# Optimization experiments

Hardware: AMD Instinct MI355X
Metric: run time of the kernel (lower is better)

## Reference

```python
import jax, jax.numpy as jnp
import numpy as np

EPS = 1e-5
H = 1024  # hidden_size
IN = 1024  # input_size
B = 4096


def _layer_norm(x, gamma, beta):
    mu = jnp.mean(x, axis=-1, keepdims=True)
    var = jnp.mean(jnp.square(x - mu), axis=-1, keepdims=True)
    return (x - mu) * jax.lax.rsqrt(var + EPS) * gamma + beta


def setup_inputs() -> dict:
    key = jax.random.key(0)
    ks = jax.random.split(key, 8)
    s_h = 1.0 / np.sqrt(H)
    s_x = 1.0 / np.sqrt(IN)
    return {
        "x": jax.random.normal(ks[0], (B, IN), dtype=jnp.float32),
        "h": jax.random.normal(ks[1], (B, H), dtype=jnp.float32),
        "c": jax.random.normal(ks[2], (B, H), dtype=jnp.float32),
        # hidden_lin: Linear(H, 4H) with bias; input_lin: Linear(IN, 4H) no bias
        "W_h": jax.random.uniform(ks[3], (H, 4 * H), jnp.float32, -s_h, s_h),
        "b_h": jax.random.uniform(ks[4], (4 * H,), jnp.float32, -s_h, s_h),
        "W_x": jax.random.uniform(ks[5], (IN, 4 * H), jnp.float32, -s_x, s_x),
        # 4 gate LayerNorms stacked [4,H], plus LayerNorm for c
        "ln_g": jnp.ones((4, H), jnp.float32),
        "ln_b": jnp.zeros((4, H), jnp.float32),
        "lnc_g": jnp.ones((H,), jnp.float32),
        "lnc_b": jnp.zeros((H,), jnp.float32),
    }


def reference(x, h, c, W_h, b_h, W_x, ln_g, ln_b, lnc_g, lnc_b):
    # ifgo = hidden_lin(h) + input_lin(x) : [B, 4H]
    ifgo = h @ W_h + b_h + x @ W_x
    ifgo = ifgo.reshape(x.shape[0], 4, H)  # [B, 4, H]
    ifgo = _layer_norm(ifgo, ln_g, ln_b)   # per-gate LayerNorm over last dim
    i, f, g, o = ifgo[:, 0], ifgo[:, 1], ifgo[:, 2], ifgo[:, 3]
    c_next = jax.nn.sigmoid(f) * c + jax.nn.sigmoid(i) * jnp.tanh(g)
    h_next = jax.nn.sigmoid(o) * jnp.tanh(_layer_norm(c_next, lnc_g, lnc_b))
    return (h_next, c_next)
```

## Files before the change

kernel.cpp:

```cpp
#include <hip/hip_runtime.h>

typedef short bf16x8 __attribute__((ext_vector_type(8)));
typedef unsigned short u16x8 __attribute__((ext_vector_type(8)));
typedef float f32x4  __attribute__((ext_vector_type(4)));

__device__ __forceinline__ float bf2f(unsigned short u) {
  union { unsigned int i; float f; } x; x.i = ((unsigned int)u) << 16; return x.f;
}
__device__ __forceinline__ unsigned short f2bf(float f) {
  union { float f; unsigned int i; } x; x.f = f;
  unsigned int r = x.i + 0x7fffu + ((x.i >> 16) & 1u);
  return (unsigned short)(r >> 16);
}
__device__ __forceinline__ float sigm(float v) { return 1.f / (1.f + __expf(-v)); }
__device__ __forceinline__ float tanh_(float v) { return 1.f - 2.f / (__expf(2.f * v) + 1.f); }
__device__ __forceinline__ int is_fp32(const void* lng) {
  return ((*(const unsigned int*)lng) & 0xFFFFu) == 0u;
}

#define AS1 __attribute__((address_space(1)))
#define AS3 __attribute__((address_space(3)))

__global__ __launch_bounds__(256) void prep_kernel(
    const void* __restrict__ h, const void* __restrict__ x,
    const void* __restrict__ Wh, const void* __restrict__ Wx,
    const void* __restrict__ lng,
    unsigned short* __restrict__ Ap, unsigned short* __restrict__ Wt)
{
  __shared__ unsigned short tile[64][65];
  const int fp = is_fp32(lng);
  if (blockIdx.x < 4096) {
    const int row = blockIdx.x;
    const int col = threadIdx.x * 8;
    const void* src; int sc;
    if (col < 1024) { src = h; sc = col; } else { src = x; sc = col - 1024; }
    u16x8 o;
    if (fp) {
      const float* s = (const float*)src + (size_t)row * 1024 + sc;
      float4 a = *(const float4*)s;
      float4 b = *(const float4*)(s + 4);
      o[0] = f2bf(a.x); o[1] = f2bf(a.y); o[2] = f2bf(a.z); o[3] = f2bf(a.w);
      o[4] = f2bf(b.x); o[5] = f2bf(b.y); o[6] = f2bf(b.z); o[7] = f2bf(b.w);
    } else {
      o = *(const u16x8*)((const unsigned short*)src + (size_t)row * 1024 + sc);
    }
    *(u16x8*)(Ap + (size_t)row * 2048 + col) = o;
  } else {
    const int bid = blockIdx.x - 4096;
    const int n0 = (bid & 63) * 64;
    const int k0 = (bid >> 6) * 64;
    const int tx = threadIdx.x & 63;
    const int ty = threadIdx.x >> 6;
    const void* src; int krow;
    if (k0 < 1024) { src = Wh; krow = k0; } else { src = Wx; krow = k0 - 1024; }
#pragma unroll
    for (int i = 0; i < 16; ++i) {
      int kk = ty + i * 4;
      size_t idx = (size_t)(krow + kk) * 4096 + n0 + tx;
      tile[kk][tx] = fp ? f2bf(((const float*)src)[idx])
                        : ((const unsigned short*)src)[idx];
    }
    __syncthreads();
#pragma unroll
    for (int i = 0; i < 16; ++i) {
      int nn = ty + i * 4;
      Wt[(size_t)(n0 + nn) * 2048 + k0 + tx] = tile[tx][nn];
    }
  }
}


#define BAR()   __builtin_amdgcn_s_barrier()
#define SBAR()  __builtin_amdgcn_sched_barrier(0)
#define LGKM0() { asm volatile("s_waitcnt lgkmcnt(0)" ::: "memory"); SBAR(); }
#define VMW(N)  { asm volatile("s_waitcnt vmcnt(" #N ")" ::: "memory"); }

#define LOAD_A(DB, MH)                                                         \
  { const unsigned short* _ba = &As[DB][(MH)*128 + wr*64 + fr][0];             \
    _Pragma("unroll") for (int mi = 0; mi < 4; ++mi)                           \
      _Pragma("unroll") for (int kh = 0; kh < 2; ++kh)                         \
        a[mi][kh] = *(const bf16x8*)(_ba + mi*1024 + ((kh*4 + fq) ^ xk) * 8); }

#define LOAD_B(DB, NH)                                                         \
  { const unsigned short* _bb = &Bs[DB][(NH)*128 + wc*32 + fr][0];             \
    _Pragma("unroll") for (int ni = 0; ni < 2; ++ni)                           \
      _Pragma("unroll") for (int kh = 0; kh < 2; ++kh)                         \
        b[ni][kh] = *(const bf16x8*)(_bb + ni*1024 + ((kh*4 + fq) ^ xk) * 8); }

#define MFMA16(MH, NH)                                                         \
  { __builtin_amdgcn_s_setprio(1);                                             \
    _Pragma("unroll") for (int kh = 0; kh < 2; ++kh)                           \
      _Pragma("unroll") for (int mi = 0; mi < 4; ++mi)                         \
        _Pragma("unroll") for (int ni = 0; ni < 2; ++ni)                       \
          acc[MH][mi][NH][ni] = __builtin_amdgcn_mfma_f32_16x16x32_bf16(       \
              a[mi][kh], b[ni][kh], acc[MH][mi][NH][ni], 0, 0, 0);             \
    __builtin_amdgcn_s_setprio(0); }

#define STAGE(G, LDS, ROW0, H, KT)                                             \
  { _Pragma("unroll") for (int l = 0; l < 2; ++l) {                            \
      const int _idx = l * 512 + tid;                                          \
      const int _r = _idx >> 3;                                                \
      const int _sg = (_idx & 7) ^ (_r & 7);                                   \
      const unsigned short* _src = (G) + (size_t)((ROW0) + (H)*128 + _r) * 2048\
                                   + ((KT) << 6) + _sg * 8;                    \
      __builtin_amdgcn_global_load_lds((const AS1 void*)_src,                  \
          (AS3 void*)(&(LDS)[0][0] + (H)*8192 + (l*512 + wave*64)*8), 16, 0, 0);\
  } }

__global__ __launch_bounds__(512, 2) void gemm_kernel(
    const unsigned short* __restrict__ Ap,
    const unsigned short* __restrict__ Wt,
    unsigned short* __restrict__ Cout)
{
  __shared__ __align__(16) unsigned short As[2][256][64];
  __shared__ __align__(16) unsigned short Bs[2][256][64];

  const int bid = blockIdx.x;
  const int swz = (bid & 7) * 32 + (bid >> 3);
  const int bm = swz >> 4, bn = swz & 15;
  const int arow = bm * 256, brow = bn * 256;

  const int tid  = threadIdx.x;
  const int wave = tid >> 6, lane = tid & 63;
  const int wr = wave >> 2, wc = wave & 3;
  const int fr = lane & 15, fq = lane >> 4;
  const int xk = fr & 7;

  f32x4 acc[2][4][2][2] = {};
  bf16x8 a[4][2], b[2][2];

  STAGE(Ap, As[0], arow, 0, 0);
  STAGE(Ap, As[0], arow, 1, 0);
  STAGE(Wt, Bs[0], brow, 0, 0);
  STAGE(Wt, Bs[0], brow, 1, 0);
  STAGE(Wt, Bs[1], brow, 0, 1);
  STAGE(Ap, As[1], arow, 1, 1);
  VMW(4);
  SBAR(); BAR();

#pragma unroll 1
  for (int it = 0; it < 16; ++it) {
    const int t1 = (2 * it + 1) & 31;
    const int t2 = (2 * it + 2) & 31;
    const int t3 = (2 * it + 3) & 31;

    LOAD_A(0, 0) LOAD_B(0, 0)
    STAGE(Ap, As[1], arow, 0, t1);
    SBAR(); BAR(); LGKM0();
    MFMA16(0, 0);
    SBAR(); BAR();
    LOAD_A(0, 1)
    STAGE(Wt, Bs[1], brow, 1, t1);
    SBAR(); BAR(); LGKM0();
    MFMA16(1, 0);
    SBAR(); BAR();
    LOAD_B(0, 1)
    STAGE(Wt, Bs[0], brow, 0, t2);
    SBAR(); BAR(); LGKM0();
    MFMA16(1, 1);
    SBAR(); BAR();
    LOAD_A(0, 0)
    STAGE(Ap, As[0], arow, 1, t2);
    SBAR(); BAR(); LGKM0();
    MFMA16(0, 1);
    VMW(4);
    SBAR(); BAR();
    LOAD_A(1, 0) LOAD_B(1, 0)
    STAGE(Ap, As[0], arow, 0, t2);
    SBAR(); BAR(); LGKM0();
    MFMA16(0, 0);
    SBAR(); BAR();
    LOAD_A(1, 1)
    STAGE(Wt, Bs[0], brow, 1, t2);
    SBAR(); BAR(); LGKM0();
    MFMA16(1, 0);
    SBAR(); BAR();
    LOAD_B(1, 1)
    STAGE(Wt, Bs[1], brow, 0, t3);
    SBAR(); BAR(); LGKM0();
    MFMA16(1, 1);
    SBAR(); BAR();
    LOAD_A(1, 0)
    STAGE(Ap, As[1], arow, 1, t3);
    SBAR(); BAR(); LGKM0();
    MFMA16(0, 1);
    VMW(4);
    SBAR(); BAR();
  }
  VMW(0);

  unsigned short* Cb = Cout + (size_t)arow * 4096 + brow;
#pragma unroll
  for (int mh = 0; mh < 2; ++mh)
#pragma unroll
    for (int mi = 0; mi < 4; ++mi)
#pragma unroll
      for (int nh = 0; nh < 2; ++nh)
#pragma unroll
        for (int ni = 0; ni < 2; ++ni) {
          const int row = mh * 128 + wr * 64 + mi * 16 + fq * 4;
          const int col = nh * 128 + wc * 32 + ni * 16 + fr;
#pragma unroll
          for (int r = 0; r < 4; ++r)
            Cb[(size_t)(row + r) * 4096 + col] = f2bf(acc[mh][mi][nh][ni][r]);
        }
}

__device__ __forceinline__ float4 load4(const void* p, size_t idx, int fp) {
  if (fp) return *(const float4*)((const float*)p + idx);
  ushort4 u = *(const ushort4*)((const unsigned short*)p + idx);
  return make_float4(bf2f(u.x), bf2f(u.y), bf2f(u.z), bf2f(u.w));
}
__device__ __forceinline__ void store4(void* p, size_t idx, int fp,
                                       float a, float b, float c, float d) {
  if (fp) {
    *(float4*)((float*)p + idx) = make_float4(a, b, c, d);
  } else {
    ushort4 u; u.x = f2bf(a); u.y = f2bf(b); u.z = f2bf(c); u.w = f2bf(d);
    *(ushort4*)((unsigned short*)p + idx) = u;
  }
}

__global__ __launch_bounds__(256) void ln_lstm_kernel(
    const unsigned short* __restrict__ parts,
    const void* __restrict__ c,
    const void* __restrict__ bh,
    const void* __restrict__ ln_g,
    const void* __restrict__ ln_b,
    const void* __restrict__ lnc_g,
    const void* __restrict__ lnc_b,
    void* __restrict__ out)
{
  const int b = blockIdx.x;
  const int t = threadIdx.x;
  const int lane = t & 63, wave = t >> 6;
  const int fp = is_fp32(lnc_g);
  const unsigned short* P0 = parts + (size_t)b * 4096;

  __shared__ float sred[4][8];

  float v[4][4];
  float red[8];
#pragma unroll
  for (int q = 0; q < 4; ++q) {
    ushort4 p0 = *(const ushort4*)(P0 + q * 1024 + t * 4);
    float4 b4 = load4(bh, q * 1024 + t * 4, fp);
    v[q][0] = bf2f(p0.x) + b4.x;
    v[q][1] = bf2f(p0.y) + b4.y;
    v[q][2] = bf2f(p0.z) + b4.z;
    v[q][3] = bf2f(p0.w) + b4.w;
    red[q * 2]     = v[q][0] + v[q][1] + v[q][2] + v[q][3];
    red[q * 2 + 1] = v[q][0]*v[q][0] + v[q][1]*v[q][1] + v[q][2]*v[q][2] + v[q][3]*v[q][3];
  }
#pragma unroll
  for (int j = 0; j < 8; ++j) {
    float s = red[j];
#pragma unroll
    for (int off = 32; off > 0; off >>= 1) s += __shfl_down(s, off, 64);
    if (lane == 0) sred[wave][j] = s;
  }
  __syncthreads();
  float mu[4], rs[4];
#pragma unroll
  for (int q = 0; q < 4; ++q) {
    float s  = sred[0][2*q]   + sred[1][2*q]   + sred[2][2*q]   + sred[3][2*q];
    float sq = sred[0][2*q+1] + sred[1][2*q+1] + sred[2][2*q+1] + sred[3][2*q+1];
    mu[q] = s * (1.f / 1024.f);
    float var = sq * (1.f / 1024.f) - mu[q] * mu[q];
    rs[q] = rsqrtf(var + 1e-5f);
  }

  float4 gI = load4(ln_g, 0 * 1024 + t * 4, fp), bI = load4(ln_b, 0 * 1024 + t * 4, fp);
  float4 gF = load4(ln_g, 1 * 1024 + t * 4, fp), bF = load4(ln_b, 1 * 1024 + t * 4, fp);
  float4 gG = load4(ln_g, 2 * 1024 + t * 4, fp), bG = load4(ln_b, 2 * 1024 + t * 4, fp);
  float4 gO = load4(ln_g, 3 * 1024 + t * 4, fp), bO = load4(ln_b, 3 * 1024 + t * 4, fp);
  float gg[4][4] = { {gI.x,gI.y,gI.z,gI.w}, {gF.x,gF.y,gF.z,gF.w},
                     {gG.x,gG.y,gG.z,gG.w}, {gO.x,gO.y,gO.z,gO.w} };
  float gb[4][4] = { {bI.x,bI.y,bI.z,bI.w}, {bF.x,bF.y,bF.z,bF.w},
                     {bG.x,bG.y,bG.z,bG.w}, {bO.x,bO.y,bO.z,bO.w} };

  float4 c4 = load4(c, (size_t)b * 1024 + t * 4, fp);
  float cin[4] = { c4.x, c4.y, c4.z, c4.w };

  float cn[4], osg[4];
  float csum = 0.f, csq = 0.f;
#pragma unroll
  for (int e = 0; e < 4; ++e) {
    float iv = (v[0][e] - mu[0]) * rs[0] * gg[0][e] + gb[0][e];
    float fv = (v[1][e] - mu[1]) * rs[1] * gg[1][e] + gb[1][e];
    float gv = (v[2][e] - mu[2]) * rs[2] * gg[2][e] + gb[2][e];
    float ov = (v[3][e] - mu[3]) * rs[3] * gg[3][e] + gb[3][e];
    float cne = sigm(fv) * cin[e] + sigm(iv) * tanh_(gv);
    cn[e] = cne; csum += cne; csq += cne * cne;
    osg[e] = sigm(ov);
  }
  store4(out, (size_t)4096 * 1024 + (size_t)b * 1024 + t * 4, fp, cn[0], cn[1], cn[2], cn[3]);

  __syncthreads();
  {
    float s0 = csum, s1 = csq;
#pragma unroll
    for (int off = 32; off > 0; off >>= 1) { s0 += __shfl_down(s0, off, 64); s1 += __shfl_down(s1, off, 64); }
    if (lane == 0) { sred[wave][0] = s0; sred[wave][1] = s1; }
  }
  __syncthreads();
  float cs   = sred[0][0] + sred[1][0] + sred[2][0] + sred[3][0];
  float csq2 = sred[0][1] + sred[1][1] + sred[2][1] + sred[3][1];
  float mu_c = cs * (1.f / 1024.f);
  float var_c = csq2 * (1.f / 1024.f) - mu_c * mu_c;
  float rs_c = rsqrtf(var_c + 1e-5f);

  float4 cg4 = load4(lnc_g, t * 4, fp);
  float4 cb4 = load4(lnc_b, t * 4, fp);

  float hn[4];
  float cgv[4] = { cg4.x, cg4.y, cg4.z, cg4.w };
  float cbv[4] = { cb4.x, cb4.y, cb4.z, cb4.w };
#pragma unroll
  for (int e = 0; e < 4; ++e)
    hn[e] = osg[e] * tanh_((cn[e] - mu_c) * rs_c * cgv[e] + cbv[e]);
  store4(out, (size_t)b * 1024 + t * 4, fp, hn[0], hn[1], hn[2], hn[3]);
}

extern "C" void kernel_launch(void* const* d_in, const int* in_sizes, int n_in,
                              void* d_out, int out_size, void* d_ws, size_t ws_size,
                              hipStream_t stream) {
  const void* x    = d_in[0];
  const void* h    = d_in[1];
  const void* c    = d_in[2];
  const void* Wh   = d_in[3];
  const void* bh   = d_in[4];
  const void* Wx   = d_in[5];
  const void* lng  = d_in[6];
  const void* lnb  = d_in[7];
  const void* lncg = d_in[8];
  const void* lncb = d_in[9];

  char* ws = (char*)d_ws;
  unsigned short* parts = (unsigned short*)ws;
  unsigned short* Wt    = (unsigned short*)(ws + (size_t)64 * 1024 * 1024);
  unsigned short* Ap    = (unsigned short*)(ws + (size_t)80 * 1024 * 1024);

  prep_kernel<<<6144, 256, 0, stream>>>(h, x, Wh, Wx, lng, Ap, Wt);
  gemm_kernel<<<256, 512, 0, stream>>>(Ap, Wt, parts);
  ln_lstm_kernel<<<4096, 256, 0, stream>>>(parts, c, bh, lng, lnb, lncg, lncb, d_out);
}
```

Baseline: 226.4 us.

## Vectorize weight transpose prep and reorder GEMM stage/MFMA quadrant schedule

The weight transpose in the prep kernel now uses vectorized float4/u16x8 global loads and 16-byte stores through an unpadded LDS tile, replacing scalar element-wise accesses. The main GEMM loop issues each global-to-LDS stage before the LDS fragment reads and visits the MFMA quadrants in a different order (00,01,11,10) so consecutive steps reuse an A or B fragment, which reduces LDS reads per step. An extra partial lgkmcnt wait is added. The unpadded transpose tile may introduce LDS bank conflicts on the column read.

New measurement: 227.0 us. Within noise of the previous version (+0.3%).

```diff
diff --git a/kernel.cpp b/kernel.cpp
--- a/kernel.cpp
+++ b/kernel.cpp
@@ -27,7 +27,7 @@
     const void* __restrict__ lng,
     unsigned short* __restrict__ Ap, unsigned short* __restrict__ Wt)
 {
-  __shared__ unsigned short tile[64][65];
+  __shared__ __align__(16) unsigned short tkn[64][64];
   const int fp = is_fp32(lng);
   if (blockIdx.x < 4096) {
     const int row = blockIdx.x;
@@ -49,22 +49,36 @@
     const int bid = blockIdx.x - 4096;
     const int n0 = (bid & 63) * 64;
     const int k0 = (bid >> 6) * 64;
-    const int tx = threadIdx.x & 63;
-    const int ty = threadIdx.x >> 6;
+    const int t = threadIdx.x;
     const void* src; int krow;
     if (k0 < 1024) { src = Wh; krow = k0; } else { src = Wx; krow = k0 - 1024; }
-#pragma unroll
-    for (int i = 0; i < 16; ++i) {
-      int kk = ty + i * 4;
-      size_t idx = (size_t)(krow + kk) * 4096 + n0 + tx;
-      tile[kk][tx] = fp ? f2bf(((const float*)src)[idx])
-                        : ((const unsigned short*)src)[idx];
+    if (fp) {
+#pragma unroll
+      for (int i = 0; i < 4; ++i) {
+        const int k  = (t >> 4) + i * 16;
+        const int n4 = (t & 15) * 4;
+        float4 w = *(const float4*)((const float*)src + (size_t)(krow + k) * 4096 + n0 + n4);
+        ushort4 u; u.x = f2bf(w.x); u.y = f2bf(w.y); u.z = f2bf(w.z); u.w = f2bf(w.w);
+        *(ushort4*)&tkn[k][n4] = u;
+      }
+    } else {
+#pragma unroll
+      for (int i = 0; i < 2; ++i) {
+        const int k  = (t >> 3) + i * 32;
+        const int n8 = (t & 7) * 8;
+        *(u16x8*)&tkn[k][n8] =
+            *(const u16x8*)((const unsigned short*)src + (size_t)(krow + k) * 4096 + n0 + n8);
+      }
     }
     __syncthreads();
 #pragma unroll
-    for (int i = 0; i < 16; ++i) {
-      int nn = ty + i * 4;
-      Wt[(size_t)(n0 + nn) * 2048 + k0 + tx] = tile[tx][nn];
+    for (int i = 0; i < 2; ++i) {
+      const int n  = (t >> 3) + i * 32;
+      const int k8 = (t & 7) * 8;
+      u16x8 o;
+#pragma unroll
+      for (int j = 0; j < 8; ++j) o[j] = tkn[k8 + j][n];
+      *(u16x8*)(Wt + (size_t)(n0 + n) * 2048 + k0 + k8) = o;
     }
   }
 }
@@ -73,6 +87,7 @@
 #define BAR()   __builtin_amdgcn_s_barrier()
 #define SBAR()  __builtin_amdgcn_sched_barrier(0)
 #define LGKM0() { asm volatile("s_waitcnt lgkmcnt(0)" ::: "memory"); SBAR(); }
+#define LGKM8() { asm volatile("s_waitcnt lgkmcnt(8)" ::: "memory"); }
 #define VMW(N)  { asm volatile("s_waitcnt vmcnt(" #N ")" ::: "memory"); }
 
 #define LOAD_A(DB, MH)                                                         \
@@ -133,8 +148,8 @@
   STAGE(Ap, As[0], arow, 1, 0);
   STAGE(Wt, Bs[0], brow, 0, 0);
   STAGE(Wt, Bs[0], brow, 1, 0);
-  STAGE(Wt, Bs[1], brow, 0, 1);
-  STAGE(Ap, As[1], arow, 1, 1);
+  STAGE(Ap, As[1], arow, 0, 1);
+  STAGE(Wt, Bs[1], brow, 1, 1);
   VMW(4);
   SBAR(); BAR();
 
@@ -144,46 +159,48 @@
     const int t2 = (2 * it + 2) & 31;
     const int t3 = (2 * it + 3) & 31;
 
+    STAGE(Wt, Bs[1], brow, 0, t1);
     LOAD_A(0, 0) LOAD_B(0, 0)
-    STAGE(Ap, As[1], arow, 0, t1);
+    LGKM8();
     SBAR(); BAR(); LGKM0();
     MFMA16(0, 0);
     SBAR(); BAR();
+    STAGE(Ap, As[1], arow, 1, t1);
+    LOAD_B(0, 1)
+    SBAR(); BAR(); LGKM0();
+    MFMA16(0, 1);
+    SBAR(); BAR();
+    STAGE(Ap, As[0], arow, 0, t2);
     LOAD_A(0, 1)
-    STAGE(Wt, Bs[1], brow, 1, t1);
+    SBAR(); BAR(); LGKM0();
+    MFMA16(1, 1);
+    SBAR(); BAR();
+    STAGE(Wt, Bs[0], brow, 1, t2);
+    LOAD_B(0, 0)
     SBAR(); BAR(); LGKM0();
     MFMA16(1, 0);
-    SBAR(); BAR();
-    LOAD_B(0, 1)
+    VMW(4);
+    SBAR(); BAR();
     STAGE(Wt, Bs[0], brow, 0, t2);
+    LOAD_A(1, 0) LOAD_B(1, 0)
+    LGKM8();
+    SBAR(); BAR(); LGKM0();
+    MFMA16(0, 0);
+    SBAR(); BAR();
+    STAGE(Ap, As[0], arow, 1, t2);
+    LOAD_B(1, 1)
+    SBAR(); BAR(); LGKM0();
+    MFMA16(0, 1);
+    SBAR(); BAR();
+    STAGE(Ap, As[1], arow, 0, t3);
+    LOAD_A(1, 1)
     SBAR(); BAR(); LGKM0();
     MFMA16(1, 1);
     SBAR(); BAR();
-    LOAD_A(0, 0)
-    STAGE(Ap, As[0], arow, 1, t2);
-    SBAR(); BAR(); LGKM0();
-    MFMA16(0, 1);
-    VMW(4);
-    SBAR(); BAR();
-    LOAD_A(1, 0) LOAD_B(1, 0)
-    STAGE(Ap, As[0], arow, 0, t2);
-    SBAR(); BAR(); LGKM0();
-    MFMA16(0, 0);
-    SBAR(); BAR();
-    LOAD_A(1, 1)
-    STAGE(Wt, Bs[0], brow, 1, t2);
+    STAGE(Wt, Bs[1], brow, 1, t3);
+    LOAD_B(1, 0)
     SBAR(); BAR(); LGKM0();
     MFMA16(1, 0);
-    SBAR(); BAR();
-    LOAD_B(1, 1)
-    STAGE(Wt, Bs[1], brow, 0, t3);
-    SBAR(); BAR(); LGKM0();
-    MFMA16(1, 1);
-    SBAR(); BAR();
-    LOAD_A(1, 0)
-    STAGE(Ap, As[1], arow, 1, t3);
-    SBAR(); BAR(); LGKM0();
-    MFMA16(0, 1);
     VMW(4);
     SBAR(); BAR();
   }
```
